# Performance work log

Hardware: AMD Instinct MI355X
Metric: run time of the kernel (lower is better)

The kernel has to match this reference:

```python
import jax, jax.numpy as jnp
import numpy as np

HEADS = 8

def conv1x1(x, w, b=None):
    # x: [b,c,h,w], w: [o,c]
    y = jnp.einsum('bchw,oc->bohw', x, w)
    if b is not None:
        y = y + b[None, :, None, None]
    return y

def dwconv3(x, w):
    # depthwise 3x3, SAME padding; w: [C,1,3,3]
    return jax.lax.conv_general_dilated(
        x, w, window_strides=(1, 1), padding='SAME',
        feature_group_count=x.shape[1],
        dimension_numbers=('NCHW', 'OIHW', 'NCHW'))

def layernorm_c(x, w, b):
    # WithBias LayerNorm over channel dim (torch normalizes last dim of b,(hw),c)
    mu = x.mean(axis=1, keepdims=True)
    var = ((x - mu) ** 2).mean(axis=1, keepdims=True)
    return (x - mu) / jnp.sqrt(var + 1e-5) * w[None, :, None, None] + b[None, :, None, None]

def l2norm_lastdim(x):
    n = jnp.sqrt(jnp.sum(x * x, axis=-1, keepdims=True))
    return x / jnp.maximum(n, 1e-12)

def channel_attention(xq, xkv, q_w, q_dw_w, kv_w, kv_dw_w, temperature, attn4, proj_w):
    b, c, h, w = xq.shape
    q = dwconv3(conv1x1(xq, q_w), q_dw_w)
    kv = dwconv3(conv1x1(xkv, kv_w), kv_dw_w)
    k, v = jnp.split(kv, 2, axis=1)
    ch = c // HEADS  # channels per head
    def heads(t):
        return t.reshape(b, HEADS, ch, h * w)
    q, k, v = heads(q), heads(k), heads(v)
    q = l2norm_lastdim(q)
    k = l2norm_lastdim(k)
    attn = jnp.einsum('bhcn,bhdn->bhcd', q, k) * temperature[None]  # [b,H,ch,ch]
    kk = int(ch * 0.9)
    thr = jax.lax.top_k(attn, kk)[0][..., -1:]
    masked = jnp.where(attn >= thr, attn, -jnp.inf)
    score = jax.nn.softmax(masked, axis=-1)
    out = jnp.einsum('bhcd,bhdn->bhcn', score, v) * attn4
    out = out.reshape(b, c, h, w)
    return conv1x1(out, proj_w)

def geglu_ffn(x, ffn_in_w, ffn_dw_w, ffn_out_w):
    y = conv1x1(x, ffn_in_w)
    y = dwconv3(y, ffn_dw_w)
    y1, y2 = jnp.split(y, 2, axis=1)
    return conv1x1(jax.nn.gelu(y1, approximate=False) * y2, ffn_out_w)


def reference(vi_featur, ir_featur, text_code,
              se_w1, se_w2, conv1x1_w, conv1x1_b, conv_out_w, conv_out_b,
              text_w1, text_b1, text_w2, text_b2,
              norm1_w, norm1_b, norm2_w, norm2_b, norm3_w, norm3_b,
              q_w, q_dw_w, kv_w, kv_dw_w, temperature, attn4, proj_w,
              ffn_in_w, ffn_dw_w, ffn_out_w):
    b, c, h, w = vi_featur.shape
    concat = jnp.concatenate([vi_featur, ir_featur], axis=1)  # [b,2c,h,w]
    squeeze = concat.mean(axis=(2, 3))                         # [b,2c]
    cw = jax.nn.sigmoid(jax.nn.relu(squeeze @ se_w1.T) @ se_w2.T)
    topk = c  # int(2*ch_dim*0.5)
    idx = jax.lax.top_k(cw, topk)[1]                           # [b,topk]
    selected = jnp.take_along_axis(concat, idx[:, :, None, None], axis=1)
    img = conv1x1(selected, conv1x1_w, conv1x1_b)              # [b,2c,h,w]
    tf = jax.nn.relu(text_code @ text_w1.T + text_b1) @ text_w2.T + text_b2  # [b,2c]
    soft_idx = jax.lax.top_k(tf, 2 * c)[1]                     # full descending perm
    shuffled = jnp.take_along_axis(img, soft_idx[:, :, None, None], axis=1)
    q_in = conv1x1(shuffled, conv_out_w, conv_out_b)           # [b,c,h,w]
    img_feature2 = conv1x1(concat, conv_out_w, conv_out_b)
    att = channel_attention(layernorm_c(q_in, norm1_w, norm1_b),
                            layernorm_c(img_feature2, norm2_w, norm2_b),
                            q_w, q_dw_w, kv_w, kv_dw_w, temperature, attn4, proj_w)
    output = att + geglu_ffn(layernorm_c(att, norm3_w, norm3_b), ffn_in_w, ffn_dw_w, ffn_out_w)
    return (output, img_feature2)


def setup_inputs() -> dict:
    key = jax.random.key(0)
    ks = jax.random.split(key, 20)
    B, C, H, W = 4, 128, 128, 128
    s = 0.05
    d = {
        'vi_featur': jax.random.normal(ks[0], (B, C, H, W), jnp.float32),
        'ir_featur': jax.random.normal(ks[1], (B, C, H, W), jnp.float32),
        'text_code': jax.random.normal(ks[2], (B, 512), jnp.float32),
        'se_w1': jax.random.normal(ks[3], (32, 256), jnp.float32) * s,
        'se_w2': jax.random.normal(ks[4], (256, 32), jnp.float32) * s,
        'conv1x1_w': jax.random.normal(ks[5], (256, 128), jnp.float32) * s,
        'conv1x1_b': jnp.zeros((256,), jnp.float32),
        'conv_out_w': jax.random.normal(ks[6], (128, 256), jnp.float32) * s,
        'conv_out_b': jnp.zeros((128,), jnp.float32),
        'text_w1': jax.random.normal(ks[7], (512, 512), jnp.float32) * s,
        'text_b1': jnp.zeros((512,), jnp.float32),
        'text_w2': jax.random.normal(ks[8], (256, 512), jnp.float32) * s,
        'text_b2': jnp.zeros((256,), jnp.float32),
        'norm1_w': jnp.ones((128,), jnp.float32), 'norm1_b': jnp.zeros((128,), jnp.float32),
        'norm2_w': jnp.ones((128,), jnp.float32), 'norm2_b': jnp.zeros((128,), jnp.float32),
        'norm3_w': jnp.ones((128,), jnp.float32), 'norm3_b': jnp.zeros((128,), jnp.float32),
        'q_w': jax.random.normal(ks[9], (128, 128), jnp.float32) * s,
        'q_dw_w': jax.random.normal(ks[10], (128, 1, 3, 3), jnp.float32) * s,
        'kv_w': jax.random.normal(ks[11], (256, 128), jnp.float32) * s,
        'kv_dw_w': jax.random.normal(ks[12], (256, 1, 3, 3), jnp.float32) * s,
        'temperature': jnp.ones((8, 1, 1), jnp.float32),
        'attn4': jnp.ones((1,), jnp.float32) * 0.2,
        'proj_w': jax.random.normal(ks[13], (128, 128), jnp.float32) * s,
        'ffn_in_w': jax.random.normal(ks[14], (680, 128), jnp.float32) * s,
        'ffn_dw_w': jax.random.normal(ks[15], (680, 1, 3, 3), jnp.float32) * s,
        'ffn_out_w': jax.random.normal(ks[16], (128, 340), jnp.float32) * s,
    }
    return d
```

## Files before the change

kernel.cpp:

```cpp
#include <hip/hip_runtime.h>

typedef unsigned short u16;
typedef __attribute__((ext_vector_type(8))) short bf16x8;
typedef __attribute__((ext_vector_type(4))) float f32x4;

#define N_PIX 16384
static constexpr long NP = 4L * 128 * N_PIX;

__device__ __forceinline__ float bf2f(u16 h) {
  unsigned u = ((unsigned)h) << 16; float f; __builtin_memcpy(&f, &u, 4); return f;
}
__device__ __forceinline__ u16 f2bf(float f) {
  unsigned u; __builtin_memcpy(&u, &f, 4);
  u = (u + 0x7fffu + ((u >> 16) & 1u)) >> 16; return (u16)u;
}

__device__ __forceinline__ float blockReduceSum256(float v) {
  #pragma unroll
  for (int o = 32; o > 0; o >>= 1) v += __shfl_down(v, o, 64);
  __shared__ float sw[4];
  int lane = threadIdx.x & 63, w = threadIdx.x >> 6;
  if (lane == 0) sw[w] = v;
  __syncthreads();
  return (threadIdx.x == 0) ? (sw[0] + sw[1] + sw[2] + sw[3]) : 0.f;
}

__global__ __launch_bounds__(256) void wconv5_k(const float* __restrict__ a0, u16* __restrict__ o0, long n0,
                                                const float* __restrict__ a1, u16* __restrict__ o1, long n1,
                                                const float* __restrict__ a2, u16* __restrict__ o2, long n2,
                                                const float* __restrict__ a3, u16* __restrict__ o3, long n3,
                                                const float* __restrict__ a4, u16* __restrict__ o4, long n4) {
  long i = (long)blockIdx.x * 256 + threadIdx.x;
  if (i < n0) o0[i] = f2bf(a0[i]);
  if (i < n1) o1[i] = f2bf(a1[i]);
  if (i < n2) o2[i] = f2bf(a2[i]);
  if (i < n3) o3[i] = f2bf(a3[i]);
  if (i < n4) o4[i] = f2bf(a4[i]);
}

__global__ __launch_bounds__(256) void squeeze_k(const float* __restrict__ vi,
                                                 const float* __restrict__ ir,
                                                 float* __restrict__ sq,
                                                 u16* __restrict__ cbf) {
  int c = blockIdx.x, b = blockIdx.y, tid = threadIdx.x;
  const float* src = (c < 128) ? (vi + ((long)b * 128 + c) * N_PIX)
                               : (ir + ((long)b * 128 + (c - 128)) * N_PIX);
  const f32x4* src4 = (const f32x4*)src;
  u16* dst = cbf + ((long)b * 256 + c) * N_PIX;
  float s = 0.f;
  #pragma unroll
  for (int j = 0; j < 8; ++j) {
    f32x4 v0 = src4[j * 512 + tid * 2];
    f32x4 v1 = src4[j * 512 + tid * 2 + 1];
    s += v0.x + v0.y + v0.z + v0.w + v1.x + v1.y + v1.z + v1.w;
    bf16x8 r;
    r[0] = (short)f2bf(v0.x); r[1] = (short)f2bf(v0.y);
    r[2] = (short)f2bf(v0.z); r[3] = (short)f2bf(v0.w);
    r[4] = (short)f2bf(v1.x); r[5] = (short)f2bf(v1.y);
    r[6] = (short)f2bf(v1.z); r[7] = (short)f2bf(v1.w);
    *(bf16x8*)(dst + j * 2048 + tid * 8) = r;
  }
  float t = blockReduceSum256(s);
  if (tid == 0) sq[b * 256 + c] = t * (1.f / 16384.f);
}

__global__ __launch_bounds__(256) void se_text1_k(const float* __restrict__ sq,
                                                  const float* __restrict__ sew1,
                                                  const float* __restrict__ sew2,
                                                  int* __restrict__ idx,
                                                  const float* __restrict__ tc,
                                                  const float* __restrict__ tw1,
                                                  const float* __restrict__ tb1,
                                                  float* __restrict__ t1f) {
  int b = blockIdx.y, tid = threadIdx.x;
  __shared__ float sm[544];
  if (blockIdx.x == 64) {
    float* s_sq = sm; float* s_h1 = sm + 256; float* s_cw = sm + 288;
    s_sq[tid] = sq[b * 256 + tid];
    __syncthreads();
    if (tid < 32) {
      float s = 0.f;
      for (int c = 0; c < 256; ++c) s += s_sq[c] * sew1[tid * 256 + c];
      s_h1[tid] = fmaxf(s, 0.f);
    }
    __syncthreads();
    {
      float s = 0.f;
      #pragma unroll
      for (int j = 0; j < 32; ++j) s += s_h1[j] * sew2[tid * 32 + j];
      s_cw[tid] = 1.f / (1.f + expf(-s));
    }
    __syncthreads();
    float my = s_cw[tid];
    int rk = 0;
    for (int c = 0; c < 256; ++c) {
      float o = s_cw[c];
      rk += (o > my) || (o == my && c < tid);
    }
    if (rk < 128) idx[b * 128 + rk] = tid;
  } else {
    float* s_tc = sm;
    int j0 = blockIdx.x * 8;
    s_tc[tid] = tc[b * 512 + tid];
    s_tc[tid + 256] = tc[b * 512 + 256 + tid];
    __syncthreads();
    int w = tid >> 6, lane = tid & 63;
    #pragma unroll
    for (int r = 0; r < 2; ++r) {
      int j = j0 + w * 2 + r;
      const float* wr = tw1 + (long)j * 512;
      float s = 0.f;
      #pragma unroll
      for (int k = 0; k < 8; ++k) s += s_tc[lane + k * 64] * wr[lane + k * 64];
      #pragma unroll
      for (int o = 32; o > 0; o >>= 1) s += __shfl_down(s, o, 64);
      if (lane == 0) t1f[b * 512 + j] = fmaxf(s + tb1[j], 0.f);
    }
  }
}

__global__ __launch_bounds__(256) void text2_k(const float* __restrict__ t1f,
                                               const float* __restrict__ tw2,
                                               const float* __restrict__ tb2,
                                               float* __restrict__ tf) {
  int b = blockIdx.y, j0 = blockIdx.x * 8, tid = threadIdx.x;
  __shared__ float s_t1[512];
  s_t1[tid] = t1f[b * 512 + tid];
  s_t1[tid + 256] = t1f[b * 512 + 256 + tid];
  __syncthreads();
  int w = tid >> 6, lane = tid & 63;
  #pragma unroll
  for (int r = 0; r < 2; ++r) {
    int j = j0 + w * 2 + r;
    const float* wr = tw2 + (long)j * 512;
    float s = 0.f;
    #pragma unroll
    for (int k = 0; k < 8; ++k) s += s_t1[lane + k * 64] * wr[lane + k * 64];
    #pragma unroll
    for (int o = 32; o > 0; o >>= 1) s += __shfl_down(s, o, 64);
    if (lane == 0) tf[b * 256 + j] = s + tb2[j];
  }
}

__global__ __launch_bounds__(256) void rank2_k(const float* __restrict__ tf,
                                               int* __restrict__ sidx) {
  int b = blockIdx.x, tid = threadIdx.x;
  __shared__ float s_tf[256];
  s_tf[tid] = tf[b * 256 + tid];
  __syncthreads();
  float my = s_tf[tid];
  int rk = 0;
  for (int c = 0; c < 256; ++c) {
    float o = s_tf[c];
    rk += (o > my) || (o == my && c < tid);
  }
  sidx[b * 256 + rk] = tid;
}

__global__ __launch_bounds__(128) void mcomb_k(const float* __restrict__ w2,
                                               const float* __restrict__ w2b,
                                               const float* __restrict__ w1,
                                               const float* __restrict__ w1b,
                                               const int* __restrict__ idx,
                                               const int* __restrict__ sidx,
                                               u16* __restrict__ mch,
                                               u16* __restrict__ mcl,
                                               float* __restrict__ bcomb) {
  int o = blockIdx.x, b = blockIdx.y, tid = threadIdx.x;
  __shared__ float s_w2[256];
  __shared__ int s_sx[256];
  s_w2[tid] = w2[o * 256 + tid];
  s_w2[tid + 128] = w2[o * 256 + tid + 128];
  s_sx[tid] = sidx[b * 256 + tid] & 255;
  s_sx[tid + 128] = sidx[b * 256 + tid + 128] & 255;
  u16* hrow = mch + ((long)b * 128 + o) * 256;
  u16* lrow = mcl + ((long)b * 128 + o) * 256;
  hrow[tid] = 0; hrow[tid + 128] = 0;
  lrow[tid] = 0; lrow[tid + 128] = 0;
  __syncthreads();
  float s = 0.f;
  for (int j = 0; j < 256; ++j) s += s_w2[j] * w1[s_sx[j] * 128 + tid];
  int cc = idx[b * 128 + tid] & 255;
  u16 hi = f2bf(s);
  hrow[cc] = hi;
  lrow[cc] = f2bf(s - bf2f(hi));
  if (tid == 0) {
    float bb = w2b[o];
    for (int j = 0; j < 256; ++j) bb += s_w2[j] * w1b[s_sx[j]];
    bcomb[b * 128 + o] = bb;
  }
}

__global__ __launch_bounds__(256) void gemm_dual_k(
    const u16* __restrict__ W2b, const float* __restrict__ b2,
    const u16* __restrict__ Mch, const u16* __restrict__ Mcl,
    const float* __restrict__ bc, const u16* __restrict__ Xb,
    float* __restrict__ out1, u16* __restrict__ qin) {
  const int N = N_PIX;
  int n0 = blockIdx.x * 64, o0 = blockIdx.y * 64, bz = blockIdx.z, tid = threadIdx.x;
  __shared__ __align__(16) u16 A1[64][72];
  __shared__ __align__(16) u16 A2h[64][72];
  __shared__ __align__(16) u16 A2l[64][72];
  __shared__ __align__(16) u16 Xs[64][72];
  f32x4 acc1[4], acc2[4];
  #pragma unroll
  for (int i = 0; i < 4; ++i) { acc1[i] = (f32x4){0,0,0,0}; acc2[i] = (f32x4){0,0,0,0}; }
  int wv = tid >> 6, lane = tid & 63;
  int lr = lane & 15, lkq = (lane >> 4) * 8;
  for (int kt = 0; kt < 4; ++kt) {
    int k0 = kt << 6;
    {
      int r = tid >> 2, o = o0 + r;
      #pragma unroll
      for (int cc = 0; cc < 2; ++cc) {
        int col = ((tid & 3) << 3) + cc * 32;
        int k = k0 + col;
        *(bf16x8*)&A1[r][col] = *(const bf16x8*)(W2b + (long)o * 256 + k);
        *(bf16x8*)&A2h[r][col] = *(const bf16x8*)(Mch + ((long)bz * 128 + o) * 256 + k);
        *(bf16x8*)&A2l[r][col] = *(const bf16x8*)(Mcl + ((long)bz * 128 + o) * 256 + k);
      }
    }
    {
      int n = tid & 63;
      const u16* src = Xb + (long)bz * 256 * N + n0 + n;
      #pragma unroll
      for (int cc = 0; cc < 2; ++cc) {
        int kb = ((tid >> 6) << 3) + cc * 32;
        int k = k0 + kb;
        bf16x8 t;
        #pragma unroll
        for (int i = 0; i < 8; ++i) t[i] = (short)src[(long)(k + i) * N];
        *(bf16x8*)&Xs[n][kb] = t;
      }
    }
    __syncthreads();
    #pragma unroll
    for (int kk = 0; kk < 2; ++kk) {
      int lk = kk * 32 + lkq;
      bf16x8 a1 = *(const bf16x8*)&A1[wv * 16 + lr][lk];
      bf16x8 a2h = *(const bf16x8*)&A2h[wv * 16 + lr][lk];
      bf16x8 a2l = *(const bf16x8*)&A2l[wv * 16 + lr][lk];
      #pragma unroll
      for (int nt = 0; nt < 4; ++nt) {
        bf16x8 bfr = *(const bf16x8*)&Xs[nt * 16 + lr][lk];
        acc1[nt] = __builtin_amdgcn_mfma_f32_16x16x32_bf16(a1, bfr, acc1[nt], 0, 0, 0);
        acc2[nt] = __builtin_amdgcn_mfma_f32_16x16x32_bf16(a2h, bfr, acc2[nt], 0, 0, 0);
        acc2[nt] = __builtin_amdgcn_mfma_f32_16x16x32_bf16(a2l, bfr, acc2[nt], 0, 0, 0);
      }
    }
    if (kt < 3) __syncthreads();
  }
  #pragma unroll
  for (int nt = 0; nt < 4; ++nt)
    #pragma unroll
    for (int r4 = 0; r4 < 4; ++r4) {
      int o = o0 + wv * 16 + (lane >> 4) * 4 + r4;
      int n = n0 + nt * 16 + (lane & 15);
      long oi = ((long)bz * 128 + o) * N + n;
      out1[oi] = acc1[nt][r4] + b2[o];
      qin[oi] = f2bf(acc2[nt][r4] + bc[bz * 128 + o]);
    }
}

template<int AMODE, int RESADD, int OUTF, int XT, int OT>
__global__ __launch_bounds__(256) void gemm_k(
    const u16* __restrict__ Ah, const u16* __restrict__ Alo, long a_bstride,
    const u16* __restrict__ X, long x_bstride,
    const u16* __restrict__ res, long res_bstride,
    void* __restrict__ outv, long out_bstride,
    int O, int K) {
  const int N = N_PIX;
  int n0 = blockIdx.x * 64;
  int o0 = blockIdx.y * 64 * OT;
  int bz = blockIdx.z;
  int tid = threadIdx.x;
  int wv = tid >> 6, lane = tid & 63;
  int lr = lane & 15, lkq = (lane >> 4) * 8;
  __shared__ __align__(16) u16 Xs[64][136];
  __shared__ __align__(16) u16 As[(XT == 3) ? 1 : 64][136];
  __shared__ __align__(16) u16 Al[(AMODE == 3) ? 64 : 1][136];
  f32x4 acc[OT][4];
  #pragma unroll
  for (int ot = 0; ot < OT; ++ot)
    #pragma unroll
    for (int i = 0; i < 4; ++i) acc[ot][i] = (f32x4){0.f, 0.f, 0.f, 0.f};

  if (XT == 3) {
    {
      int n = tid >> 2, koff = (tid & 3) << 5;
      const u16* src = X + (long)bz * x_bstride + (long)(n0 + n) * 128 + koff;
      #pragma unroll
      for (int j = 0; j < 4; ++j)
        *(bf16x8*)&Xs[n][koff + j * 8] = *(const bf16x8*)(src + j * 8);
    }
    __syncthreads();
    #pragma unroll
    for (int ot = 0; ot < OT; ++ot) {
      int oc = o0 + ot * 64 + wv * 16 + lr;
      if (oc > O - 1) oc = O - 1;
      const u16* Arow = Ah + (long)oc * 128;
      bf16x8 afr[4];
      #pragma unroll
      for (int kk = 0; kk < 4; ++kk) afr[kk] = *(const bf16x8*)(Arow + kk * 32 + lkq);
      #pragma unroll
      for (int kk = 0; kk < 4; ++kk) {
        int lk = kk * 32 + lkq;
        #pragma unroll
        for (int nt = 0; nt < 4; ++nt) {
          bf16x8 bfr = *(const bf16x8*)&Xs[nt * 16 + lr][lk];
          acc[ot][nt] = __builtin_amdgcn_mfma_f32_16x16x32_bf16(afr[kk], bfr, acc[ot][nt], 0, 0, 0);
        }
      }
    }
    __syncthreads();
  } else {
    int nk = XT ? 1 : ((K + 127) >> 7);
    for (int kt = 0; kt < nk; ++kt) {
      int k0 = kt << 7;
      if (XT == 1) {
        int n = tid >> 2, koff = (tid & 3) << 5;
        const u16* src = X + (long)bz * x_bstride + (long)(n0 + n) * 128 + koff;
        #pragma unroll
        for (int j = 0; j < 4; ++j)
          *(bf16x8*)&Xs[n][koff + j * 8] = *(const bf16x8*)(src + j * 8);
      } else {
        int n = tid & 63;
        const u16* src = X + (long)bz * x_bstride + n0 + n;
        #pragma unroll
        for (int cc = 0; cc < 4; ++cc) {
          int kb = ((tid >> 6) << 3) + cc * 32;
          int k = k0 + kb;
          bf16x8 t;
          #pragma unroll
          for (int i = 0; i < 8; ++i)
            t[i] = (short)((k + i < K) ? src[(long)(k + i) * N] : (u16)0);
          *(bf16x8*)&Xs[n][kb] = t;
        }
      }
      #pragma unroll
      for (int ot = 0; ot < OT; ++ot) {
        {
          int r = tid >> 2, o = o0 + ot * 64 + r;
          #pragma unroll
          for (int cc = 0; cc < 4; ++cc) {
            int col = ((tid & 3) << 3) + cc * 32;
            int k = k0 + col;
            if (AMODE == 2) {
              bf16x8 t;
              if (o < O && k + 8 <= K) {
                t = *(const bf16x8*)(Ah + (long)o * K + k);
              } else {
                #pragma unroll
                for (int i = 0; i < 8; ++i)
                  t[i] = (short)((o < O && k + i < K) ? Ah[(long)o * K + k + i] : (u16)0);
              }
              *(bf16x8*)&As[r][col] = t;
            } else {
              long base = (long)bz * a_bstride + (long)o * K + k;
              *(bf16x8*)&As[r][col] = *(const bf16x8*)(Ah + base);
              *(bf16x8*)&Al[r][col] = *(const bf16x8*)(Alo + base);
            }
          }
        }
        __syncthreads();
        #pragma unroll
        for (int kk = 0; kk < 4; ++kk) {
          int lk = kk * 32 + lkq;
          bf16x8 afr = *(const bf16x8*)&As[wv * 16 + lr][lk];
          bf16x8 alr;
          if (AMODE == 3) alr = *(const bf16x8*)&Al[wv * 16 + lr][lk];
          #pragma unroll
          for (int nt = 0; nt < 4; ++nt) {
            bf16x8 bfr = *(const bf16x8*)&Xs[nt * 16 + lr][lk];
            acc[ot][nt] = __builtin_amdgcn_mfma_f32_16x16x32_bf16(afr, bfr, acc[ot][nt], 0, 0, 0);
            if (AMODE == 3)
              acc[ot][nt] = __builtin_amdgcn_mfma_f32_16x16x32_bf16(alr, bfr, acc[ot][nt], 0, 0, 0);
          }
        }
        __syncthreads();
      }
    }
  }

  #pragma unroll
  for (int ot = 0; ot < OT; ++ot) {
    if (ot > 0) __syncthreads();
    if (OUTF == 0) {
      u16* st = &Xs[0][0];
      #pragma unroll
      for (int nt = 0; nt < 4; ++nt)
        #pragma unroll
        for (int r4 = 0; r4 < 4; ++r4) {
          int row = wv * 16 + (lane >> 4) * 4 + r4;
          int col = nt * 16 + (lane & 15);
          st[row * 68 + col] = f2bf(acc[ot][nt][r4]);
        }
      __syncthreads();
      #pragma unroll
      for (int it = 0; it < 2; ++it) {
        int row = (tid >> 3) + it * 32;
        int col = (tid & 7) * 8;
        int o = o0 + ot * 64 + row;
        if (o < O) {
          bf16x8 v = *(bf16x8*)&st[row * 68 + col];
          *(bf16x8*)((u16*)outv + (long)bz * out_bstride + (long)o * N + n0 + col) = v;
        }
      }
    } else {
      float* st = (float*)&Xs[0][0];
      #pragma unroll
      for (int nt = 0; nt < 4; ++nt)
        #pragma unroll
        for (int r4 = 0; r4 < 4; ++r4) {
          int row = wv * 16 + (lane >> 4) * 4 + r4;
          int col = nt * 16 + (lane & 15);
          st[row * 68 + col] = acc[ot][nt][r4];
        }
      __syncthreads();
      {
        int row = tid >> 2, colb = (tid & 3) * 16;
        int o = o0 + ot * 64 + row;
        if (o < O) {
          float* dst = (float*)outv + (long)bz * out_bstride + (long)o * N + n0 + colb;
          bf16x8 rv0, rv1;
          if (RESADD) {
            const u16* rp = res + (long)bz * res_bstride + (long)o * N + n0 + colb;
            rv0 = *(const bf16x8*)rp;
            rv1 = *(const bf16x8*)(rp + 8);
          }
          #pragma unroll
          for (int j = 0; j < 4; ++j) {
            f32x4 v = *(f32x4*)&st[row * 68 + colb + j * 4];
            if (RESADD) {
              #pragma unroll
              for (int i = 0; i < 4; ++i) {
                int idx = j * 4 + i;
                u16 rr = (u16)((idx < 8) ? rv0[idx] : rv1[idx - 8]);
                v[i] += bf2f(rr);
              }
            }
            *(f32x4*)(dst + j * 4) = v;
          }
        }
      }
    }
  }
}

__global__ __launch_bounds__(256) void ln12t_k(const u16* __restrict__ qin,
                                               const float* __restrict__ o1,
                                               const float* __restrict__ g1,
                                               const float* __restrict__ b1,
                                               const float* __restrict__ g2,
                                               const float* __restrict__ b2,
                                               u16* __restrict__ xqT,
                                               u16* __restrict__ xkvT) {
  int p0 = blockIdx.x * 64, y = blockIdx.y, tid = threadIdx.x;
  bool second = (y >= 4);
  int b = second ? y - 4 : y;
  const float* gamma = second ? g2 : g1;
  const float* beta  = second ? b2 : b1;
  u16* outT = second ? xkvT : xqT;
  int px = tid & 63, g4 = tid >> 6;
  __shared__ float tile[128][65];
  __shared__ float red[8][64];
  __shared__ float gmm[128], bta[128], mu_s[64], rs_s[64];
  if (tid < 128) { gmm[tid] = gamma[tid]; bta[tid] = beta[tid]; }
  long bofs = (long)b * 128 * N_PIX;
  float s = 0.f;
  for (int c = g4; c < 128; c += 4) {
    long ix = bofs + (long)c * N_PIX + p0 + px;
    float v = second ? o1[ix] : bf2f(qin[ix]);
    tile[c][px] = v;
    s += v;
  }
  red[g4][px] = s;
  __syncthreads();
  if (g4 == 0) mu_s[px] = (red[0][px] + red[1][px] + red[2][px] + red[3][px]) * (1.f / 128.f);
  __syncthreads();
  float mu = mu_s[px];
  float s2 = 0.f;
  for (int c = g4; c < 128; c += 4) { float d = tile[c][px] - mu; s2 += d * d; }
  red[4 + g4][px] = s2;
  __syncthreads();
  if (g4 == 0) {
    float var = (red[4][px] + red[5][px] + red[6][px] + red[7][px]) * (1.f / 128.f);
    rs_s[px] = rsqrtf(var + 1e-5f);
  }
  __syncthreads();
  float rs = rs_s[px];
  for (int c = g4; c < 128; c += 4)
    tile[c][px] = (tile[c][px] - mu) * rs * gmm[c] + bta[c];
  __syncthreads();
  int px2 = tid >> 2, c0 = (tid & 3) << 5;
  u16* dst = outT + ((long)b * N_PIX + p0 + px2) * 128 + c0;
  #pragma unroll
  for (int j = 0; j < 4; ++j) {
    bf16x8 r;
    #pragma unroll
    for (int i = 0; i < 8; ++i) r[i] = (short)f2bf(tile[c0 + j * 8 + i][px2]);
    *(bf16x8*)(dst + j * 8) = r;
  }
}

__global__ __launch_bounds__(256) void lnt_k(const u16* __restrict__ in,
                                             const float* __restrict__ gamma,
                                             const float* __restrict__ beta,
                                             u16* __restrict__ outT) {
  int p0 = blockIdx.x * 64, b = blockIdx.y, tid = threadIdx.x;
  int px = tid & 63, g4 = tid >> 6;
  __shared__ float tile[128][65];
  __shared__ float red[8][64];
  __shared__ float gmm[128], bta[128], mu_s[64], rs_s[64];
  if (tid < 128) { gmm[tid] = gamma[tid]; bta[tid] = beta[tid]; }
  long bofs = (long)b * 128 * N_PIX;
  float s = 0.f;
  for (int c = g4; c < 128; c += 4) {
    float v = bf2f(in[bofs + (long)c * N_PIX + p0 + px]);
    tile[c][px] = v;
    s += v;
  }
  red[g4][px] = s;
  __syncthreads();
  if (g4 == 0) mu_s[px] = (red[0][px] + red[1][px] + red[2][px] + red[3][px]) * (1.f / 128.f);
  __syncthreads();
  float mu = mu_s[px];
  float s2 = 0.f;
  for (int c = g4; c < 128; c += 4) { float d = tile[c][px] - mu; s2 += d * d; }
  red[4 + g4][px] = s2;
  __syncthreads();
  if (g4 == 0) {
    float var = (red[4][px] + red[5][px] + red[6][px] + red[7][px]) * (1.f / 128.f);
    rs_s[px] = rsqrtf(var + 1e-5f);
  }
  __syncthreads();
  float rs = rs_s[px];
  for (int c = g4; c < 128; c += 4)
    tile[c][px] = (tile[c][px] - mu) * rs * gmm[c] + bta[c];
  __syncthreads();
  int px2 = tid >> 2, c0 = (tid & 3) << 5;
  u16* dst = outT + ((long)b * N_PIX + p0 + px2) * 128 + c0;
  #pragma unroll
  for (int j = 0; j < 4; ++j) {
    bf16x8 r;
    #pragma unroll
    for (int i = 0; i < 8; ++i) r[i] = (short)f2bf(tile[c0 + j * 8 + i][px2]);
    *(bf16x8*)(dst + j * 8) = r;
  }
}

__global__ __launch_bounds__(256) void dw3t2_k(const u16* __restrict__ inQ,
                                               const float* __restrict__ wQ,
                                               u16* __restrict__ outQ,
                                               const u16* __restrict__ inKV,
                                               const float* __restrict__ wKV,
                                               u16* __restrict__ outKV) {
  int gp = blockIdx.x >> 3, stripe = blockIdx.x & 7, tid = threadIdx.x;
  const u16* in; const float* w; u16* out; int c; long pbase;
  if (gp < 512) { in = inQ;  w = wQ;  out = outQ;  c = gp & 127;  pbase = (long)gp * N_PIX; }
  else { int p2 = gp - 512; in = inKV; w = wKV; out = outKV; c = p2 & 255; pbase = (long)p2 * N_PIX; }
  int y0 = stripe * 16;
  __shared__ __align__(16) u16 tile[18][136];
  for (int v = tid; v < 288; v += 256) {
    int r = v >> 4, col = (v & 15) << 3;
    int y = y0 - 1 + r;
    bf16x8 t;
    #pragma unroll
    for (int i = 0; i < 8; ++i) t[i] = 0;
    if (y >= 0 && y < 128) t = *(const bf16x8*)(in + pbase + y * 128 + col);
    *(bf16x8*)&tile[r][col] = t;
  }
  float wv[9];
  #pragma unroll
  for (int j = 0; j < 9; ++j) wv[j] = w[c * 9 + j];
  __syncthreads();
  int row = tid >> 4, col0 = (tid & 15) << 3;
  float a[3][10];
  #pragma unroll
  for (int dr = 0; dr < 3; ++dr)
    #pragma unroll
    for (int i = 0; i < 10; ++i) {
      int x = col0 - 1 + i;
      a[dr][i] = (x >= 0 && x < 128) ? bf2f(tile[row + dr][x]) : 0.f;
    }
  bf16x8 res;
  #pragma unroll
  for (int j = 0; j < 8; ++j) {
    float s = 0.f;
    #pragma unroll
    for (int dr = 0; dr < 3; ++dr)
      #pragma unroll
      for (int dx = 0; dx < 3; ++dx) s += wv[dr * 3 + dx] * a[dr][j + dx];
    res[j] = (short)f2bf(s);
  }
  *(bf16x8*)(out + pbase + (y0 + row) * 128 + col0) = res;
}

__global__ __launch_bounds__(256) void dw3gelu4_k(const u16* __restrict__ ft,
                                                  const float* __restrict__ w,
                                                  u16* __restrict__ fg) {
  int plane = blockIdx.x >> 3, stripe = blockIdx.x & 7, tid = threadIdx.x;
  int b = plane / 340, c = plane % 340;
  const u16* t1 = ft + ((long)b * 680 + c) * N_PIX;
  const u16* t2 = ft + ((long)b * 680 + 340 + c) * N_PIX;
  u16* g = fg + ((long)b * 340 + c) * N_PIX;
  int y0 = stripe * 16;
  __shared__ __align__(16) u16 ta[18][136];
  __shared__ __align__(16) u16 tb[18][136];
  for (int v = tid; v < 288; v += 256) {
    int r = v >> 4, col = (v & 15) << 3;
    int y = y0 - 1 + r;
    bf16x8 u1, u2;
    #pragma unroll
    for (int i = 0; i < 8; ++i) { u1[i] = 0; u2[i] = 0; }
    if (y >= 0 && y < 128) {
      u1 = *(const bf16x8*)(t1 + y * 128 + col);
      u2 = *(const bf16x8*)(t2 + y * 128 + col);
    }
    *(bf16x8*)&ta[r][col] = u1;
    *(bf16x8*)&tb[r][col] = u2;
  }
  float w1[9], w2[9];
  #pragma unroll
  for (int j = 0; j < 9; ++j) { w1[j] = w[c * 9 + j]; w2[j] = w[(340 + c) * 9 + j]; }
  __syncthreads();
  int row = tid >> 4, col0 = (tid & 15) << 3;
  float a[3][10], bb[3][10];
  #pragma unroll
  for (int dr = 0; dr < 3; ++dr)
    #pragma unroll
    for (int i = 0; i < 10; ++i) {
      int x = col0 - 1 + i;
      bool ok = (x >= 0 && x < 128);
      a[dr][i] = ok ? bf2f(ta[row + dr][x]) : 0.f;
      bb[dr][i] = ok ? bf2f(tb[row + dr][x]) : 0.f;
    }
  bf16x8 res;
  #pragma unroll
  for (int j = 0; j < 8; ++j) {
    float s1 = 0.f, s2 = 0.f;
    #pragma unroll
    for (int dr = 0; dr < 3; ++dr)
      #pragma unroll
      for (int dx = 0; dx < 3; ++dx) {
        s1 += w1[dr * 3 + dx] * a[dr][j + dx];
        s2 += w2[dr * 3 + dx] * bb[dr][j + dx];
      }
    float gl = 0.5f * s1 * (1.f + erff(s1 * 0.70710678118f));
    res[j] = (short)f2bf(gl * s2);
  }
  *(bf16x8*)(g + (y0 + row) * 128 + col0) = res;
}

__global__ __launch_bounds__(256) void rownorm2_k(const u16* __restrict__ q,
                                                  const u16* __restrict__ kv,
                                                  float* __restrict__ qn,
                                                  float* __restrict__ kn) {
  int x = blockIdx.x, b = blockIdx.y, tid = threadIdx.x;
  const u16* src;
  float* dst;
  if (x < 128) { src = q + (long)b * 128 * N_PIX + (long)x * N_PIX; dst = qn + b * 128 + x; }
  else { int r = x - 128; src = kv + (long)b * 256 * N_PIX + (long)r * N_PIX; dst = kn + b * 128 + r; }
  float s = 0.f;
  #pragma unroll
  for (int j = 0; j < 8; ++j) {
    bf16x8 v = *(const bf16x8*)(src + j * 2048 + tid * 8);
    #pragma unroll
    for (int i = 0; i < 8; ++i) { float f = bf2f((u16)v[i]); s += f * f; }
  }
  float t = blockReduceSum256(s);
  if (tid == 0) *dst = sqrtf(t);
}

__global__ __launch_bounds__(256) void attn_part_k(const u16* __restrict__ q,
                                                   const u16* __restrict__ kbase,
                                                   long kbstride,
                                                   float* __restrict__ part) {
  int ch = blockIdx.x, h = blockIdx.y, b = blockIdx.z, tid = threadIdx.x;
  int n0 = ch * 256;
  __shared__ __align__(16) u16 qc[16][280];
  __shared__ __align__(16) u16 kc[16][280];
  #pragma unroll
  for (int j = 0; j < 2; ++j) {
    int v = tid + j * 256;
    int r = v >> 5, col = (v & 31) << 3;
    *(bf16x8*)&qc[r][col] = *(const bf16x8*)(q + ((long)b * 128 + h * 16 + r) * N_PIX + n0 + col);
    *(bf16x8*)&kc[r][col] = *(const bf16x8*)(kbase + (long)b * kbstride + (long)(h * 16 + r) * N_PIX + n0 + col);
  }
  __syncthreads();
  int c = tid >> 4, d = tid & 15;
  float acc = 0.f;
  #pragma unroll 4
  for (int nb = 0; nb < 32; ++nb) {
    bf16x8 qv = *(const bf16x8*)&qc[c][nb * 8];
    bf16x8 kv = *(const bf16x8*)&kc[d][nb * 8];
    #pragma unroll
    for (int i = 0; i < 8; ++i) acc += bf2f((u16)qv[i]) * bf2f((u16)kv[i]);
  }
  part[(long)((((b * 8 + h) * 16 + c) * 16 + d)) * 64 + ch] = acc;
}

__global__ __launch_bounds__(256) void attn_reduce_k(const float* __restrict__ part,
                                                     const float* __restrict__ qn,
                                                     const float* __restrict__ kn,
                                                     const float* __restrict__ temp,
                                                     float* __restrict__ attnm) {
  int idx = blockIdx.x * 256 + threadIdx.x;
  const float* p = part + (long)idx * 64;
  float s = 0.f;
  #pragma unroll
  for (int j = 0; j < 64; ++j) s += p[j];
  int d = idx & 15, c = (idx >> 4) & 15, h = (idx >> 8) & 7, b = idx >> 11;
  float nq = fmaxf(qn[b * 128 + h * 16 + c], 1e-12f);
  float nk = fmaxf(kn[b * 128 + h * 16 + d], 1e-12f);
  attnm[idx] = s / (nq * nk) * temp[h];
}

__global__ __launch_bounds__(128) void score_cmb_k(const float* __restrict__ attnm,
                                                   const float* __restrict__ projw,
                                                   const float* __restrict__ attn4p,
                                                   u16* __restrict__ cmbh,
                                                   u16* __restrict__ cmbl) {
  int b = blockIdx.x, tid = threadIdx.x;
  __shared__ float att_s[2048], score_s[2048];
  for (int i = tid; i < 2048; i += 128) att_s[i] = attnm[(long)b * 2048 + i];
  __syncthreads();
  {
    int h = tid >> 4, c = tid & 15;
    float v[16], t[16];
    #pragma unroll
    for (int d = 0; d < 16; ++d) { v[d] = att_s[(h * 16 + c) * 16 + d]; t[d] = v[d]; }
    float thr = 0.f, M = -1e30f;
    for (int it = 0; it < 14; ++it) {
      float m = -1e30f; int mi = 0;
      #pragma unroll
      for (int d = 0; d < 16; ++d) if (t[d] > m) { m = t[d]; mi = d; }
      if (it == 0) M = m;
      thr = m;
      t[mi] = -1e31f;
    }
    float s = 0.f, e[16];
    #pragma unroll
    for (int d = 0; d < 16; ++d) { e[d] = (v[d] >= thr) ? expf(v[d] - M) : 0.f; s += e[d]; }
    float inv = 1.f / s;
    #pragma unroll
    for (int d = 0; d < 16; ++d) score_s[(h * 16 + c) * 16 + d] = e[d] * inv;
  }
  __syncthreads();
  float a4 = attn4p[0];
  int o = tid;
  for (int hd = 0; hd < 128; ++hd) {
    int h = hd >> 4, d = hd & 15;
    float s = 0.f;
    #pragma unroll
    for (int c = 0; c < 16; ++c)
      s += projw[o * 128 + h * 16 + c] * score_s[(h * 16 + c) * 16 + d];
    float v = a4 * s;
    long oi = ((long)b * 128 + o) * 128 + hd;
    u16 hi = f2bf(v);
    cmbh[oi] = hi;
    cmbl[oi] = f2bf(v - bf2f(hi));
  }
}

extern "C" void kernel_launch(void* const* d_in, const int* in_sizes, int n_in,
                              void* d_out, int out_size, void* d_ws, size_t ws_size,
                              hipStream_t stream) {
  (void)in_sizes; (void)n_in; (void)out_size; (void)ws_size;
  const float* vi        = (const float*)d_in[0];
  const float* ir        = (const float*)d_in[1];
  const float* text_code = (const float*)d_in[2];
  const float* se_w1     = (const float*)d_in[3];
  const float* se_w2     = (const float*)d_in[4];
  const float* conv1x1_w = (const float*)d_in[5];
  const float* conv1x1_b = (const float*)d_in[6];
  const float* conv_out_w= (const float*)d_in[7];
  const float* conv_out_b= (const float*)d_in[8];
  const float* text_w1   = (const float*)d_in[9];
  const float* text_b1   = (const float*)d_in[10];
  const float* text_w2   = (const float*)d_in[11];
  const float* text_b2   = (const float*)d_in[12];
  const float* norm1_w   = (const float*)d_in[13];
  const float* norm1_b   = (const float*)d_in[14];
  const float* norm2_w   = (const float*)d_in[15];
  const float* norm2_b   = (const float*)d_in[16];
  const float* norm3_w   = (const float*)d_in[17];
  const float* norm3_b   = (const float*)d_in[18];
  const float* q_w       = (const float*)d_in[19];
  const float* q_dw_w    = (const float*)d_in[20];
  const float* kv_w      = (const float*)d_in[21];
  const float* kv_dw_w   = (const float*)d_in[22];
  const float* temperature = (const float*)d_in[23];
  const float* attn4     = (const float*)d_in[24];
  const float* proj_w    = (const float*)d_in[25];
  const float* ffn_in_w  = (const float*)d_in[26];
  const float* ffn_dw_w  = (const float*)d_in[27];
  const float* ffn_out_w = (const float*)d_in[28];
  float* out0 = (float*)d_out;
  float* out1 = out0 + NP;

  char* W = (char*)d_ws;
  float* sq_f  = (float*)(W + 0);
  int*   idx_i = (int*)(W + 4096);
  int*   sidx_i= (int*)(W + 6144);
  u16*   Mch   = (u16*)(W + 12288);
  u16*   Mcl   = (u16*)(W + 274432);
  float* bcomb = (float*)(W + 536576);
  float* qn_f  = (float*)(W + 538624);
  float* kn_f  = (float*)(W + 540672);
  float* attnm = (float*)(W + 542720);
  u16*   cmbh  = (u16*)(W + 575488);
  u16*   cmbl  = (u16*)(W + 706560);
  float* t1f   = (float*)(W + 834560);
  float* tf_f  = (float*)(W + 842752);
  u16*   W2b   = (u16*)(W + 846848);
  u16*   qwb   = (u16*)(W + 912384);
  u16*   kvwb  = (u16*)(W + 945152);
  u16*   ffnWb = (u16*)(W + (1 << 20));
  u16*   ffnOb = (u16*)(W + (1 << 20) + 174080);
  u16* S    = (u16*)(W + (2 << 20));
  u16* CC   = S;
  u16* KD   = S + 512L * N_PIX;
  u16* KVD  = S + 1024L * N_PIX;
  u16* CBF  = S + 1024L * N_PIX;
  u16* XQT  = S + 2048L * N_PIX;
  u16* X3T  = S + 2048L * N_PIX;
  u16* XKVT = S + 2560L * N_PIX;
  u16* FT4  = S + 2560L * N_PIX;
  u16* FG4  = S + 5280L * N_PIX;
  u16* KVT  = (u16*)out0;
  u16* ATT  = KD;

  const long SN = 128L * N_PIX;
  const long SN2 = 256L * N_PIX;

  wconv5_k<<<340, 256, 0, stream>>>(conv_out_w, W2b, 32768, q_w, qwb, 16384,
                                    kv_w, kvwb, 32768, ffn_in_w, ffnWb, 87040,
                                    ffn_out_w, ffnOb, 43520);
  squeeze_k<<<dim3(256, 4), 256, 0, stream>>>(vi, ir, sq_f, CBF);
  se_text1_k<<<dim3(65, 4), 256, 0, stream>>>(sq_f, se_w1, se_w2, idx_i,
                                              text_code, text_w1, text_b1, t1f);
  text2_k<<<dim3(32, 4), 256, 0, stream>>>(t1f, text_w2, text_b2, tf_f);
  rank2_k<<<4, 256, 0, stream>>>(tf_f, sidx_i);
  mcomb_k<<<dim3(128, 4), 128, 0, stream>>>(conv_out_w, conv_out_b, conv1x1_w,
                                            conv1x1_b, idx_i, sidx_i, Mch, Mcl, bcomb);
  gemm_dual_k<<<dim3(256, 2, 4), 256, 0, stream>>>(
      W2b, conv_out_b, Mch, Mcl, bcomb, CBF, out1, CC);
  ln12t_k<<<dim3(256, 8), 256, 0, stream>>>(CC, out1, norm1_w, norm1_b,
                                            norm2_w, norm2_b, XQT, XKVT);
  gemm_k<2, 0, 0, 3, 2><<<dim3(256, 1, 4), 256, 0, stream>>>(
      qwb, nullptr, 0, XQT, SN, nullptr, 0, KD, SN, 128, 128);
  gemm_k<2, 0, 0, 3, 2><<<dim3(256, 2, 4), 256, 0, stream>>>(
      kvwb, nullptr, 0, XKVT, SN, nullptr, 0, KVT, SN2, 256, 128);
  dw3t2_k<<<12288, 256, 0, stream>>>(KD, q_dw_w, CC, KVT, kv_dw_w, KVD);
  rownorm2_k<<<dim3(256, 4), 256, 0, stream>>>(CC, KVD, qn_f, kn_f);
  float* part = (float*)out0;
  attn_part_k<<<dim3(64, 8, 4), 256, 0, stream>>>(CC, KVD, SN2, part);
  attn_reduce_k<<<32, 256, 0, stream>>>(part, qn_f, kn_f, temperature, attnm);
  score_cmb_k<<<4, 128, 0, stream>>>(attnm, proj_w, attn4, cmbh, cmbl);
  gemm_k<3, 0, 0, 0, 2><<<dim3(256, 1, 4), 256, 0, stream>>>(
      cmbh, cmbl, 128L * 128, KVD + SN, SN2, nullptr, 0, ATT, SN, 128, 128);
  lnt_k<<<dim3(256, 4), 256, 0, stream>>>(ATT, norm3_w, norm3_b, X3T);
  gemm_k<2, 0, 0, 3, 2><<<dim3(256, 6, 4), 256, 0, stream>>>(
      ffnWb, nullptr, 0, X3T, SN, nullptr, 0, FT4, 680L * N_PIX, 680, 128);
  dw3gelu4_k<<<10880, 256, 0, stream>>>(FT4, ffn_dw_w, FG4);
  gemm_k<2, 1, 1, 0, 2><<<dim3(256, 1, 4), 256, 0, stream>>>(
      ffnOb, nullptr, 0, FG4, 340L * N_PIX, ATT, SN,
      out0, SN, 128, 340);
}
```

Baseline: 388.6 us.

## Emit pixel-major bf16 from dual GEMM and replace transposing LayerNorm with in-place row LN

The dual GEMM now stages its outputs in shared memory. Besides the fp32 out1, it writes two pixel-major (transposed) bf16 tensors: the query input and a bf16 copy of out1. The old ln12t kernel, which read the channel-major qin and fp32 out1 and transposed through shared memory, is replaced by a simple per-pixel row LayerNorm that normalizes these buffers in place. This cuts the fp32 re-read and the separate transpose pass, and drops the unused XT==1 load path. In exchange, LN2 now sees bf16-rounded inputs and uses a one-pass E[x²]−μ² variance, which slightly changes numerics.

```diff
diff --git a/kernel.cpp b/kernel.cpp
--- a/kernel.cpp
+++ b/kernel.cpp
@@ -195,13 +195,14 @@
     const u16* __restrict__ W2b, const float* __restrict__ b2,
     const u16* __restrict__ Mch, const u16* __restrict__ Mcl,
     const float* __restrict__ bc, const u16* __restrict__ Xb,
-    float* __restrict__ out1, u16* __restrict__ qin) {
+    float* __restrict__ out1, u16* __restrict__ qinT, u16* __restrict__ img2T) {
   const int N = N_PIX;
   int n0 = blockIdx.x * 64, o0 = blockIdx.y * 64, bz = blockIdx.z, tid = threadIdx.x;
-  __shared__ __align__(16) u16 A1[64][72];
-  __shared__ __align__(16) u16 A2h[64][72];
-  __shared__ __align__(16) u16 A2l[64][72];
-  __shared__ __align__(16) u16 Xs[64][72];
+  __shared__ __align__(16) char smem[36864];
+  u16* A1  = (u16*)smem;
+  u16* A2h = (u16*)(smem + 9216);
+  u16* A2l = (u16*)(smem + 18432);
+  u16* Xs  = (u16*)(smem + 27648);
   f32x4 acc1[4], acc2[4];
   #pragma unroll
   for (int i = 0; i < 4; ++i) { acc1[i] = (f32x4){0,0,0,0}; acc2[i] = (f32x4){0,0,0,0}; }
@@ -215,9 +216,9 @@
       for (int cc = 0; cc < 2; ++cc) {
         int col = ((tid & 3) << 3) + cc * 32;
         int k = k0 + col;
-        *(bf16x8*)&A1[r][col] = *(const bf16x8*)(W2b + (long)o * 256 + k);
-        *(bf16x8*)&A2h[r][col] = *(const bf16x8*)(Mch + ((long)bz * 128 + o) * 256 + k);
-        *(bf16x8*)&A2l[r][col] = *(const bf16x8*)(Mcl + ((long)bz * 128 + o) * 256 + k);
+        *(bf16x8*)&A1[r * 72 + col] = *(const bf16x8*)(W2b + (long)o * 256 + k);
+        *(bf16x8*)&A2h[r * 72 + col] = *(const bf16x8*)(Mch + ((long)bz * 128 + o) * 256 + k);
+        *(bf16x8*)&A2l[r * 72 + col] = *(const bf16x8*)(Mcl + ((long)bz * 128 + o) * 256 + k);
       }
     }
     {
@@ -230,36 +231,90 @@
         bf16x8 t;
         #pragma unroll
         for (int i = 0; i < 8; ++i) t[i] = (short)src[(long)(k + i) * N];
-        *(bf16x8*)&Xs[n][kb] = t;
+        *(bf16x8*)&Xs[n * 72 + kb] = t;
       }
     }
     __syncthreads();
     #pragma unroll
     for (int kk = 0; kk < 2; ++kk) {
       int lk = kk * 32 + lkq;
-      bf16x8 a1 = *(const bf16x8*)&A1[wv * 16 + lr][lk];
-      bf16x8 a2h = *(const bf16x8*)&A2h[wv * 16 + lr][lk];
-      bf16x8 a2l = *(const bf16x8*)&A2l[wv * 16 + lr][lk];
+      bf16x8 a1 = *(const bf16x8*)&A1[(wv * 16 + lr) * 72 + lk];
+      bf16x8 a2h = *(const bf16x8*)&A2h[(wv * 16 + lr) * 72 + lk];
+      bf16x8 a2l = *(const bf16x8*)&A2l[(wv * 16 + lr) * 72 + lk];
       #pragma unroll
       for (int nt = 0; nt < 4; ++nt) {
-        bf16x8 bfr = *(const bf16x8*)&Xs[nt * 16 + lr][lk];
+        bf16x8 bfr = *(const bf16x8*)&Xs[(nt * 16 + lr) * 72 + lk];
         acc1[nt] = __builtin_amdgcn_mfma_f32_16x16x32_bf16(a1, bfr, acc1[nt], 0, 0, 0);
         acc2[nt] = __builtin_amdgcn_mfma_f32_16x16x32_bf16(a2h, bfr, acc2[nt], 0, 0, 0);
         acc2[nt] = __builtin_amdgcn_mfma_f32_16x16x32_bf16(a2l, bfr, acc2[nt], 0, 0, 0);
       }
     }
-    if (kt < 3) __syncthreads();
-  }
+    __syncthreads();
+  }
+  float* st1 = (float*)smem;
+  u16*  stq = (u16*)(smem + 17408);
+  u16*  sti = (u16*)(smem + 26112);
   #pragma unroll
   for (int nt = 0; nt < 4; ++nt)
     #pragma unroll
     for (int r4 = 0; r4 < 4; ++r4) {
-      int o = o0 + wv * 16 + (lane >> 4) * 4 + r4;
-      int n = n0 + nt * 16 + (lane & 15);
-      long oi = ((long)bz * 128 + o) * N + n;
-      out1[oi] = acc1[nt][r4] + b2[o];
-      qin[oi] = f2bf(acc2[nt][r4] + bc[bz * 128 + o]);
-    }
+      int o_l = wv * 16 + (lane >> 4) * 4 + r4;
+      int n_l = nt * 16 + (lane & 15);
+      float v1 = acc1[nt][r4] + b2[o0 + o_l];
+      float v2 = acc2[nt][r4] + bc[bz * 128 + o0 + o_l];
+      st1[o_l * 68 + n_l] = v1;
+      stq[n_l * 68 + o_l] = f2bf(v2);
+      sti[n_l * 68 + o_l] = f2bf(v1);
+    }
+  __syncthreads();
+  {
+    int row = tid >> 2, colb = (tid & 3) * 16;
+    float* dst = out1 + ((long)bz * 128 + o0 + row) * N + n0 + colb;
+    #pragma unroll
+    for (int j = 0; j < 4; ++j)
+      *(f32x4*)(dst + j * 4) = *(f32x4*)&st1[row * 68 + colb + j * 4];
+    u16* dq = qinT + ((long)bz * N_PIX + n0 + row) * 128 + o0 + colb;
+    u16* di = img2T + ((long)bz * N_PIX + n0 + row) * 128 + o0 + colb;
+    *(bf16x8*)dq = *(bf16x8*)&stq[row * 68 + colb];
+    *(bf16x8*)(dq + 8) = *(bf16x8*)&stq[row * 68 + colb + 8];
+    *(bf16x8*)di = *(bf16x8*)&sti[row * 68 + colb];
+    *(bf16x8*)(di + 8) = *(bf16x8*)&sti[row * 68 + colb + 8];
+  }
+}
+
+__global__ __launch_bounds__(256) void lnrow_k(u16* __restrict__ t0, u16* __restrict__ t1,
+                                               const float* __restrict__ g1, const float* __restrict__ b1,
+                                               const float* __restrict__ g2, const float* __restrict__ b2) {
+  int y = blockIdx.y, tid = threadIdx.x;
+  u16* buf = y ? t1 : t0;
+  const float* g = y ? g2 : g1;
+  const float* bb = y ? b2 : b1;
+  __shared__ float gs[128], bs[128];
+  if (tid < 128) { gs[tid] = g[tid]; bs[tid] = bb[tid]; }
+  __syncthreads();
+  long p = (long)blockIdx.x * 256 + tid;
+  u16* src = buf + p * 128;
+  bf16x8 v[16];
+  float sum = 0.f, sq = 0.f;
+  #pragma unroll
+  for (int j = 0; j < 16; ++j) {
+    v[j] = *(const bf16x8*)(src + j * 8);
+    #pragma unroll
+    for (int i = 0; i < 8; ++i) { float f = bf2f((u16)v[j][i]); sum += f; sq += f * f; }
+  }
+  float mu = sum * (1.f / 128.f);
+  float var = sq * (1.f / 128.f) - mu * mu;
+  float rs = rsqrtf(fmaxf(var, 0.f) + 1e-5f);
+  #pragma unroll
+  for (int j = 0; j < 16; ++j) {
+    bf16x8 r;
+    #pragma unroll
+    for (int i = 0; i < 8; ++i) {
+      float f = bf2f((u16)v[j][i]);
+      r[i] = (short)f2bf((f - mu) * rs * gs[j * 8 + i] + bs[j * 8 + i]);
+    }
+    *(bf16x8*)(src + j * 8) = r;
+  }
 }
 
 template<int AMODE, int RESADD, int OUTF, int XT, int OT>
@@ -314,16 +369,10 @@
     }
     __syncthreads();
   } else {
-    int nk = XT ? 1 : ((K + 127) >> 7);
+    int nk = (K + 127) >> 7;
     for (int kt = 0; kt < nk; ++kt) {
       int k0 = kt << 7;
-      if (XT == 1) {
-        int n = tid >> 2, koff = (tid & 3) << 5;
-        const u16* src = X + (long)bz * x_bstride + (long)(n0 + n) * 128 + koff;
-        #pragma unroll
-        for (int j = 0; j < 4; ++j)
-          *(bf16x8*)&Xs[n][koff + j * 8] = *(const bf16x8*)(src + j * 8);
-      } else {
+      {
         int n = tid & 63;
         const u16* src = X + (long)bz * x_bstride + n0 + n;
         #pragma unroll
@@ -447,62 +496,6 @@
   }
 }
 
-__global__ __launch_bounds__(256) void ln12t_k(const u16* __restrict__ qin,
-                                               const float* __restrict__ o1,
-                                               const float* __restrict__ g1,
-                                               const float* __restrict__ b1,
-                                               const float* __restrict__ g2,
-                                               const float* __restrict__ b2,
-                                               u16* __restrict__ xqT,
-                                               u16* __restrict__ xkvT) {
-  int p0 = blockIdx.x * 64, y = blockIdx.y, tid = threadIdx.x;
-  bool second = (y >= 4);
-  int b = second ? y - 4 : y;
-  const float* gamma = second ? g2 : g1;
-  const float* beta  = second ? b2 : b1;
-  u16* outT = second ? xkvT : xqT;
-  int px = tid & 63, g4 = tid >> 6;
-  __shared__ float tile[128][65];
-  __shared__ float red[8][64];
-  __shared__ float gmm[128], bta[128], mu_s[64], rs_s[64];
-  if (tid < 128) { gmm[tid] = gamma[tid]; bta[tid] = beta[tid]; }
-  long bofs = (long)b * 128 * N_PIX;
-  float s = 0.f;
-  for (int c = g4; c < 128; c += 4) {
-    long ix = bofs + (long)c * N_PIX + p0 + px;
-    float v = second ? o1[ix] : bf2f(qin[ix]);
-    tile[c][px] = v;
-    s += v;
-  }
-  red[g4][px] = s;
-  __syncthreads();
-  if (g4 == 0) mu_s[px] = (red[0][px] + red[1][px] + red[2][px] + red[3][px]) * (1.f / 128.f);
-  __syncthreads();
-  float mu = mu_s[px];
-  float s2 = 0.f;
-  for (int c = g4; c < 128; c += 4) { float d = tile[c][px] - mu; s2 += d * d; }
-  red[4 + g4][px] = s2;
-  __syncthreads();
-  if (g4 == 0) {
-    float var = (red[4][px] + red[5][px] + red[6][px] + red[7][px]) * (1.f / 128.f);
-    rs_s[px] = rsqrtf(var + 1e-5f);
-  }
-  __syncthreads();
-  float rs = rs_s[px];
-  for (int c = g4; c < 128; c += 4)
-    tile[c][px] = (tile[c][px] - mu) * rs * gmm[c] + bta[c];
-  __syncthreads();
-  int px2 = tid >> 2, c0 = (tid & 3) << 5;
-  u16* dst = outT + ((long)b * N_PIX + p0 + px2) * 128 + c0;
-  #pragma unroll
-  for (int j = 0; j < 4; ++j) {
-    bf16x8 r;
-    #pragma unroll
-    for (int i = 0; i < 8; ++i) r[i] = (short)f2bf(tile[c0 + j * 8 + i][px2]);
-    *(bf16x8*)(dst + j * 8) = r;
-  }
-}
-
 __global__ __launch_bounds__(256) void lnt_k(const u16* __restrict__ in,
                                              const float* __restrict__ gamma,
                                              const float* __restrict__ beta,
@@ -823,7 +816,6 @@
   u16* KD   = S + 512L * N_PIX;
   u16* KVD  = S + 1024L * N_PIX;
   u16* CBF  = S + 1024L * N_PIX;
-  u16* XQT  = S + 2048L * N_PIX;
   u16* X3T  = S + 2048L * N_PIX;
   u16* XKVT = S + 2560L * N_PIX;
   u16* FT4  = S + 2560L * N_PIX;
@@ -845,11 +837,10 @@
   mcomb_k<<<dim3(128, 4), 128, 0, stream>>>(conv_out_w, conv_out_b, conv1x1_w,
                                             conv1x1_b, idx_i, sidx_i, Mch, Mcl, bcomb);
   gemm_dual_k<<<dim3(256, 2, 4), 256, 0, stream>>>(
-      W2b, conv_out_b, Mch, Mcl, bcomb, CBF, out1, CC);
-  ln12t_k<<<dim3(256, 8), 256, 0, stream>>>(CC, out1, norm1_w, norm1_b,
-                                            norm2_w, norm2_b, XQT, XKVT);
+      W2b, conv_out_b, Mch, Mcl, bcomb, CBF, out1, CC, XKVT);
+  lnrow_k<<<dim3(256, 2), 256, 0, stream>>>(CC, XKVT, norm1_w, norm1_b, norm2_w, norm2_b);
   gemm_k<2, 0, 0, 3, 2><<<dim3(256, 1, 4), 256, 0, stream>>>(
-      qwb, nullptr, 0, XQT, SN, nullptr, 0, KD, SN, 128, 128);
+      qwb, nullptr, 0, CC, SN, nullptr, 0, KD, SN, 128, 128);
   gemm_k<2, 0, 0, 3, 2><<<dim3(256, 2, 4), 256, 0, stream>>>(
       kvwb, nullptr, 0, XKVT, SN, nullptr, 0, KVT, SN2, 256, 128);
   dw3t2_k<<<12288, 256, 0, stream>>>(KD, q_dw_w, CC, KVT, kv_dw_w, KVD);
```

Measured after the change: 390.4 us. No clear change (+0.5%).
